# Performance work log

Measured on AMD Instinct MI355X. Metric: run time of the kernel, lower is better.

## Reference

```python
import jax, jax.numpy as jnp
import numpy as np

N, E, IN_DIM, HID, HEADS = 50000, 800000, 128, 16, 8
EPS_BN = 1e-5


def _gat_conv(x, edge_index, W, att_src, att_dst, bias, heads, out_ch, concat):
    # x: [N, F_in]; W: [heads*out_ch, F_in]; att_*: [heads, out_ch]
    n = x.shape[0]
    h = (x @ W.T).reshape(n, heads, out_ch)            # [N, H, C]
    a_src = (h * att_src[None]).sum(-1)                # [N, H]
    a_dst = (h * att_dst[None]).sum(-1)                # [N, H]
    src, dst = edge_index[0], edge_index[1]
    alpha = jax.nn.leaky_relu(a_src[src] + a_dst[dst], negative_slope=0.2)  # [E, H]
    # segment softmax over destination node (per head)
    amax = jax.ops.segment_max(alpha, dst, num_segments=n)
    amax = jnp.where(jnp.isfinite(amax), amax, 0.0)
    ex = jnp.exp(alpha - amax[dst])
    denom = jax.ops.segment_sum(ex, dst, num_segments=n)
    attn = ex / (denom[dst] + 1e-16)                   # [E, H]
    msg = h[src] * attn[:, :, None]                    # [E, H, C]
    out = jax.ops.segment_sum(msg, dst, num_segments=n)  # [N, H, C]
    out = out.reshape(n, heads * out_ch) if concat else out.mean(axis=1)
    return out + bias


def _bn_eval(h, mean, var, gamma, beta):
    return (h - mean) * jax.lax.rsqrt(var + EPS_BN) * gamma + beta


def setup_inputs() -> dict:
    key = jax.random.key(0)
    ks = jax.random.split(key, 16)
    s = 0.1
    inp = {
        "x": jax.random.normal(ks[0], (N, IN_DIM), jnp.float32),
        "edge_index": jax.random.randint(ks[1], (2, E), 0, N, jnp.int32),
        # layer 0: GATConv(128 -> 16, heads=8, concat)
        "w0": jax.random.normal(ks[2], (HEADS * HID, IN_DIM), jnp.float32) * s,
        "asrc0": jax.random.normal(ks[3], (HEADS, HID), jnp.float32) * s,
        "adst0": jax.random.normal(ks[4], (HEADS, HID), jnp.float32) * s,
        "b0": jnp.zeros((HEADS * HID,), jnp.float32),
        "skip0": jax.random.normal(ks[5], (HEADS * HID, IN_DIM), jnp.float32) * s,
        "bn0_g": jnp.ones((HEADS * HID,), jnp.float32),
        "bn0_b": jnp.zeros((HEADS * HID,), jnp.float32),
        "bn0_m": jax.random.normal(ks[6], (HEADS * HID,), jnp.float32) * s,
        "bn0_v": jax.random.uniform(ks[7], (HEADS * HID,), jnp.float32, 0.5, 1.5),
        # layer 1: GATConv(128 -> 16, heads=1, concat=False)
        "w1": jax.random.normal(ks[8], (HID, HEADS * HID), jnp.float32) * s,
        "asrc1": jax.random.normal(ks[9], (1, HID), jnp.float32) * s,
        "adst1": jax.random.normal(ks[10], (1, HID), jnp.float32) * s,
        "b1": jnp.zeros((HID,), jnp.float32),
        "skip1": jax.random.normal(ks[11], (HID, HEADS * HID), jnp.float32) * s,
        "bn1_g": jnp.ones((HID,), jnp.float32),
        "bn1_b": jnp.zeros((HID,), jnp.float32),
        "bn1_m": jax.random.normal(ks[12], (HID,), jnp.float32) * s,
        "bn1_v": jax.random.uniform(ks[13], (HID,), jnp.float32, 0.5, 1.5),
    }
    return inp


def reference(x, edge_index, w0, asrc0, adst0, b0, skip0, bn0_g, bn0_b, bn0_m, bn0_v,
              w1, asrc1, adst1, b1, skip1, bn1_g, bn1_b, bn1_m, bn1_v):
    # eval mode: dropout = identity, BN uses running stats
    h_in = x
    h = _gat_conv(h_in, edge_index, w0, asrc0, adst0, b0, HEADS, HID, True)   # [N, 128]
    h = _bn_eval(h, bn0_m, bn0_v, bn0_g, bn0_b)
    h = h + h_in @ skip0.T
    h = jax.nn.elu(h)
    h_in = h
    h = _gat_conv(h_in, edge_index, w1, asrc1, adst1, b1, 1, HID, False)      # [N, 16]
    h = _bn_eval(h, bn1_m, bn1_v, bn1_g, bn1_b)
    h = h + h_in @ skip1.T
    h = jax.nn.elu(h)
    return h
```

## Files before the change

kernel.cpp:

```cpp
#include <hip/hip_runtime.h>
#include <hip/hip_bf16.h>

#define NN 50000
#define EE 800000
#define INDIM 128
#define HIDC 16
#define NHEAD 8
#define COARSE 196
#define EPB 2048
#define CAPR 6144
#define CAPB 8192
#define CVT_BLKS 37

typedef __attribute__((ext_vector_type(8))) short bf16x8;
typedef __attribute__((ext_vector_type(4))) float f32x4;

__device__ __forceinline__ float bf2f(unsigned short u) {
    union { float f; unsigned int i; } v; v.i = ((unsigned int)u) << 16; return v.f;
}
__device__ __forceinline__ unsigned short f2bf(float f) {
    union { float f; unsigned int i; } v; v.f = f;
    unsigned int r = v.i + 0x7FFFu + ((v.i >> 16) & 1u);
    return (unsigned short)(r >> 16);
}

__global__ __launch_bounds__(256) void k_prep(
    const float* __restrict__ w0, const float* __restrict__ skip0,
    const float* __restrict__ w1, const float* __restrict__ skip1,
    const float* __restrict__ b0, const float* __restrict__ g0,
    const float* __restrict__ bb0, const float* __restrict__ m0,
    const float* __restrict__ v0,
    const float* __restrict__ b1, const float* __restrict__ g1,
    const float* __restrict__ bb1, const float* __restrict__ m1,
    const float* __restrict__ v1,
    unsigned int* __restrict__ wb2, unsigned int* __restrict__ wb1_2,
    float2* __restrict__ acb0, float2* __restrict__ acb1,
    const int* __restrict__ ei, int* __restrict__ ccur0,
    unsigned int* __restrict__ pairs)
{
    if (blockIdx.x < CVT_BLKS) {
        const long NW = 256 * 128 / 4;
        const long NW1 = 32 * 128 / 4;
        long i = (long)blockIdx.x * 256 + threadIdx.x;
        if (i < NW) {
            const float4* src = (i < 128 * 128 / 4) ? ((const float4*)w0 + i)
                                                    : ((const float4*)skip0 + (i - 128 * 128 / 4));
            float4 v = *src;
            wb2[i * 2]     = (unsigned int)f2bf(v.x) | ((unsigned int)f2bf(v.y) << 16);
            wb2[i * 2 + 1] = (unsigned int)f2bf(v.z) | ((unsigned int)f2bf(v.w) << 16);
        } else if (i < NW + NW1) {
            long j = i - NW;
            const float4* src = (j < 16 * 128 / 4) ? ((const float4*)w1 + j)
                                                   : ((const float4*)skip1 + (j - 16 * 128 / 4));
            float4 v = *src;
            wb1_2[j * 2]     = (unsigned int)f2bf(v.x) | ((unsigned int)f2bf(v.y) << 16);
            wb1_2[j * 2 + 1] = (unsigned int)f2bf(v.z) | ((unsigned int)f2bf(v.w) << 16);
        } else if (i < NW + NW1 + 128) {
            int c = (int)(i - NW - NW1);
            float A = g0[c] * rsqrtf(v0[c] + 1e-5f);
            acb0[c] = make_float2(A, (b0[c] - m0[c]) * A + bb0[c]);
        } else if (i < NW + NW1 + 128 + 16) {
            int c = (int)(i - NW - NW1 - 128);
            float A = g1[c] * rsqrtf(v1[c] + 1e-5f);
            acb1[c] = make_float2(A, (b1[c] - m1[c]) * A + bb1[c]);
        }
        return;
    }

    __shared__ int bcnt[256];
    __shared__ int lofs[256];
    __shared__ int gofs[256];
    __shared__ unsigned int stage[EPB];
    __shared__ int gpos[EPB];
    const int t = threadIdx.x;
    const int e0 = (blockIdx.x - CVT_BLKS) * EPB;

    bcnt[t] = 0;
    __syncthreads();

    int mybin[8], myrank[8];
    unsigned int mypair[8];
    #pragma unroll
    for (int k = 0; k < 8; k++) {
        int e = e0 + k * 256 + t;
        mybin[k] = -1;
        if (e < EE) {
            int s = ei[e], d = ei[EE + e];
            int b = d >> 8;
            myrank[k] = atomicAdd(&bcnt[b], 1);
            mybin[k] = b;
            mypair[k] = ((unsigned)d << 16) | (unsigned)s;
        }
    }
    __syncthreads();

    int v = bcnt[t];
    lofs[t] = v;
    __syncthreads();
    for (int off = 1; off < 256; off <<= 1) {
        int u = (t >= off) ? lofs[t - off] : 0;
        __syncthreads();
        lofs[t] += u;
        __syncthreads();
    }
    if (t < COARSE && v > 0)
        gofs[t] = t * CAPR + atomicAdd(&ccur0[t], v);
    __syncthreads();

    #pragma unroll
    for (int k = 0; k < 8; k++) {
        int b = mybin[k];
        if (b >= 0) {
            int slot = (lofs[b] - bcnt[b]) + myrank[k];
            stage[slot] = mypair[k];
            gpos[slot]  = gofs[b] + myrank[k];
        }
    }
    __syncthreads();

    const int total = lofs[255];
    for (int i = t; i < total; i += 256)
        pairs[gpos[i]] = stage[i];
}

__global__ __launch_bounds__(256) void k_mid(
    const unsigned int* __restrict__ pairs, const int* __restrict__ ccur0,
    unsigned short* __restrict__ srcidx, int* __restrict__ rowbeg,
    int* __restrict__ deg,
    const float* __restrict__ x, const unsigned short* __restrict__ wb,
    const float* __restrict__ asrc0, const float* __restrict__ adst0,
    unsigned char* __restrict__ h0f, unsigned short* __restrict__ s0b,
    float* __restrict__ a_src0, float* __restrict__ a_dst0)
{
    __shared__ int fcnt[256], fofs[256], fcur[256];
    __shared__ unsigned short stage[CAPB];

    if (blockIdx.x < COARSE) {
        const int b = blockIdx.x, t = threadIdx.x;
        const int beg = b * CAPR;
        int cnt = ccur0[b];
        if (cnt > CAPR) cnt = CAPR;

        fcnt[t] = 0;
        __syncthreads();
        for (int i = t; i < cnt; i += 256) {
            unsigned int d = pairs[beg + i] >> 16;
            atomicAdd(&fcnt[d & 255], 1);
        }
        __syncthreads();

        int v = fcnt[t];
        fofs[t] = v;
        __syncthreads();
        for (int off = 1; off < 256; off <<= 1) {
            int u = (t >= off) ? fofs[t - off] : 0;
            __syncthreads();
            fofs[t] += u;
            __syncthreads();
        }
        int ex = fofs[t] - v;
        int node = b * 256 + t;
        if (node < NN) { rowbeg[node] = beg + ex; deg[node] = v; }
        fcur[t] = ex;
        __syncthreads();

        for (int i = t; i < cnt; i += 256) {
            unsigned int p = pairs[beg + i];
            unsigned int d = p >> 16;
            int slot = atomicAdd(&fcur[d & 255], 1);
            stage[slot] = (unsigned short)(p & 0xFFFFu);
        }
        __syncthreads();
        for (int i = t; i < cnt; i += 256)
            srcidx[beg + i] = stage[i];
        return;
    }

    const int bid = blockIdx.x - COARSE;
    const int wave = threadIdx.x >> 6;
    const int lane = threadIdx.x & 63;
    const int lrow = lane & 15;
    const int quad = lane >> 4;
    const int rowbase = bid * 32;

    bf16x8 afrag[2][4];
    #pragma unroll
    for (int sub = 0; sub < 2; sub++) {
        const int row = min(rowbase + sub * 16 + lrow, NN - 1);
        const float* xr = x + (long)row * 128;
        #pragma unroll
        for (int ki = 0; ki < 4; ki++) {
            float4 a = *(const float4*)(xr + ki * 32 + quad * 8);
            float4 b = *(const float4*)(xr + ki * 32 + quad * 8 + 4);
            bf16x8 f;
            f[0] = (short)f2bf(a.x); f[1] = (short)f2bf(a.y);
            f[2] = (short)f2bf(a.z); f[3] = (short)f2bf(a.w);
            f[4] = (short)f2bf(b.x); f[5] = (short)f2bf(b.y);
            f[6] = (short)f2bf(b.z); f[7] = (short)f2bf(b.w);
            afrag[sub][ki] = f;
        }
    }

    #pragma unroll
    for (int t = 0; t < 4; t++) {
        const int jg = wave * 64 + t * 16 + lrow;
        bf16x8 bfrag[4];
        #pragma unroll
        for (int ki = 0; ki < 4; ki++)
            bfrag[ki] = *(const bf16x8*)(wb + (long)jg * 128 + ki * 32 + quad * 8);
        float4 asv = {0.f, 0.f, 0.f, 0.f}, adv = {0.f, 0.f, 0.f, 0.f};
        if (wave < 2) {
            const int cb = wave * 64 + t * 16 + quad * 4;
            asv = *(const float4*)(asrc0 + cb);
            adv = *(const float4*)(adst0 + cb);
        }
        #pragma unroll
        for (int sub = 0; sub < 2; sub++) {
            f32x4 acc = (f32x4){0.f, 0.f, 0.f, 0.f};
            #pragma unroll
            for (int ki = 0; ki < 4; ki++)
                acc = __builtin_amdgcn_mfma_f32_16x16x32_bf16(bfrag[ki], afrag[sub][ki], acc, 0, 0, 0);

            const int node = rowbase + sub * 16 + lrow;
            if (node < NN) {
                if (wave < 2) {
                    const int cb = wave * 64 + t * 16 + quad * 4;
                    unsigned int u = __builtin_amdgcn_cvt_pk_fp8_f32(acc[0], acc[1], 0u, 0);
                    u = __builtin_amdgcn_cvt_pk_fp8_f32(acc[2], acc[3], u, 1);
                    *(unsigned int*)(h0f + (long)node * 128 + cb) = u;
                    float ps = acc[0] * asv.x + acc[1] * asv.y + acc[2] * asv.z + acc[3] * asv.w;
                    float pd = acc[0] * adv.x + acc[1] * adv.y + acc[2] * adv.z + acc[3] * adv.w;
                    ps += __shfl_xor(ps, 16); ps += __shfl_xor(ps, 32);
                    pd += __shfl_xor(pd, 16); pd += __shfl_xor(pd, 32);
                    if (quad == 0) {
                        const int h = wave * 4 + t;
                        a_src0[(long)node * 8 + h] = ps;
                        a_dst0[(long)node * 8 + h] = pd;
                    }
                } else {
                    const int cb = (wave - 2) * 64 + t * 16 + quad * 4;
                    uint2 u;
                    u.x = (unsigned int)f2bf(acc[0]) | ((unsigned int)f2bf(acc[1]) << 16);
                    u.y = (unsigned int)f2bf(acc[2]) | ((unsigned int)f2bf(acc[3]) << 16);
                    *(uint2*)(s0b + (long)node * 128 + cb) = u;
                }
            }
        }
    }
}

__global__ __launch_bounds__(256) void k_agg0(
    const int* __restrict__ rowbeg, const int* __restrict__ deg,
    const unsigned short* __restrict__ srcidx,
    const unsigned char* __restrict__ h0f, const float* __restrict__ a_src0,
    const float* __restrict__ a_dst0, const unsigned short* __restrict__ s0b,
    const float2* __restrict__ acb0, unsigned int* __restrict__ hab2)
{
    const int d = (blockIdx.x * 256 + threadIdx.x) >> 6;
    if (d >= NN) return;
    const int lane = threadIdx.x & 63;
    const int beg = rowbeg[d], end = beg + deg[d];
    const int eslot = lane >> 3;
    const int hph1 = lane & 7;
    const int c = lane * 2;
    const int hsel = lane >> 3;
    const float adst = a_dst0[(long)d * 8 + hph1];

    float den = 0.f;
    float2 accA = {0.f, 0.f}, accB = {0.f, 0.f};
    for (int i = beg; i < end; i += 16) {
        const int idxA = i + eslot;
        const int idxB = i + 8 + eslot;
        const bool vA = idxA < end;
        const bool vB = idxB < end;
        const int sA = vA ? (int)srcidx[idxA] : 0;
        const int sB = vB ? (int)srcidx[idxB] : 0;
        float aA = a_src0[(long)sA * 8 + hph1] + adst;
        float aB = a_src0[(long)sB * 8 + hph1] + adst;
        aA = aA > 0.f ? aA : 0.2f * aA;
        aB = aB > 0.f ? aB : 0.2f * aB;
        const float wA = vA ? __expf(aA) : 0.f;
        const float wB = vB ? __expf(aB) : 0.f;
        den += wA + wB;
        #pragma unroll
        for (int j = 0; j < 8; j++) {
            const float wjA = __shfl(wA, j * 8 + hsel);
            const int sjA = __shfl(sA, j * 8);
            const float wjB = __shfl(wB, j * 8 + hsel);
            const int sjB = __shfl(sB, j * 8);
            const unsigned int uA = *(const unsigned short*)(h0f + (long)sjA * 128 + c);
            const unsigned int uB = *(const unsigned short*)(h0f + (long)sjB * 128 + c);
            accA.x += wjA * __builtin_amdgcn_cvt_f32_fp8(uA, 0);
            accA.y += wjA * __builtin_amdgcn_cvt_f32_fp8(uA, 1);
            accB.x += wjB * __builtin_amdgcn_cvt_f32_fp8(uB, 0);
            accB.y += wjB * __builtin_amdgcn_cvt_f32_fp8(uB, 1);
        }
    }
    float2 acc = {accA.x + accB.x, accA.y + accB.y};
    den += __shfl_xor(den, 8);
    den += __shfl_xor(den, 16);
    den += __shfl_xor(den, 32);
    const float denh = __shfl(den, hsel);
    const float inv = 1.f / (denh + 1e-16f);

    const float4 ab = *(const float4*)((const float*)acb0 + 2 * c);
    const unsigned int s0u = *(const unsigned int*)(s0b + (long)d * 128 + c);
    float x0 = acc.x * inv * ab.x + ab.y + bf2f((unsigned short)s0u);
    float x1 = acc.y * inv * ab.z + ab.w + bf2f((unsigned short)(s0u >> 16));
    x0 = x0 > 0.f ? x0 : __expf(x0) - 1.f;
    x1 = x1 > 0.f ? x1 : __expf(x1) - 1.f;
    hab2[(long)d * 64 + lane] =
        (unsigned int)f2bf(x0) | ((unsigned int)f2bf(x1) << 16);
}

__global__ __launch_bounds__(256) void k_post0(
    const unsigned short* __restrict__ hab,
    const unsigned short* __restrict__ wb1,
    const float* __restrict__ asrc1, const float* __restrict__ adst1,
    unsigned short* __restrict__ h1b, float* __restrict__ s1,
    float* __restrict__ a_src1, float* __restrict__ a_dst1)
{
    const int tid = threadIdx.x;
    const int lane = tid & 63, wave = tid >> 6;
    const int lrow = lane & 15, quad = lane >> 4;

    bf16x8 bfrag[2][4];
    #pragma unroll
    for (int t = 0; t < 2; t++)
        #pragma unroll
        for (int ki = 0; ki < 4; ki++)
            bfrag[t][ki] = *(const bf16x8*)(wb1 + (long)(t * 16 + lrow) * 128 + ki * 32 + quad * 8);
    const float avec = asrc1[lrow];
    const float dvec = adst1[lrow];

    const int tile = blockIdx.x * 4 + wave;
    if (tile * 16 >= NN) return;
    const int n0 = tile * 16;
    const long arow = (long)(n0 + lrow) * 128;

    bf16x8 afrag[4];
    #pragma unroll
    for (int ki = 0; ki < 4; ki++)
        afrag[ki] = *(const bf16x8*)(hab + arow + ki * 32 + quad * 8);

    f32x4 acc0 = (f32x4){0.f, 0.f, 0.f, 0.f};
    f32x4 acc1 = (f32x4){0.f, 0.f, 0.f, 0.f};
    #pragma unroll
    for (int ki = 0; ki < 4; ki++) {
        acc0 = __builtin_amdgcn_mfma_f32_16x16x32_bf16(afrag[ki], bfrag[0][ki], acc0, 0, 0, 0);
        acc1 = __builtin_amdgcn_mfma_f32_16x16x32_bf16(afrag[ki], bfrag[1][ki], acc1, 0, 0, 0);
    }

    #pragma unroll
    for (int r = 0; r < 4; r++) {
        const int node = n0 + quad * 4 + r;
        h1b[(long)node * 16 + lrow] = f2bf(acc0[r]);
        s1[(long)node * 16 + lrow] = acc1[r];
        float ps = acc0[r] * avec;
        float pd = acc0[r] * dvec;
        ps += __shfl_xor(ps, 1); ps += __shfl_xor(ps, 2);
        ps += __shfl_xor(ps, 4); ps += __shfl_xor(ps, 8);
        pd += __shfl_xor(pd, 1); pd += __shfl_xor(pd, 2);
        pd += __shfl_xor(pd, 4); pd += __shfl_xor(pd, 8);
        if (lrow == 0) { a_src1[node] = ps; a_dst1[node] = pd; }
    }
}

__global__ __launch_bounds__(256) void k_agg1_final(
    const int* __restrict__ rowbeg, const int* __restrict__ deg,
    const unsigned short* __restrict__ srcidx,
    const unsigned short* __restrict__ h1b, const float* __restrict__ a_src1,
    const float* __restrict__ a_dst1, const float* __restrict__ s1,
    const float2* __restrict__ acb1, float* __restrict__ out)
{
    const int gid = blockIdx.x * 256 + threadIdx.x;
    const int d = gid >> 3;
    if (d >= NN) return;
    const int lane = threadIdx.x & 63;
    const int gl = lane & 7;
    const int gb = lane & ~7;
    const int c0 = gl * 2;
    const int beg = rowbeg[d], end = beg + deg[d];
    const float adst = a_dst1[d];

    float den = 0.f;
    float2 accA = {0.f, 0.f}, accB = {0.f, 0.f};
    for (int i = beg; i < end; i += 16) {
        const int idxA = i + gl;
        const int idxB = i + 8 + gl;
        const bool vA = idxA < end;
        const bool vB = idxB < end;
        const int sA = vA ? (int)srcidx[idxA] : 0;
        const int sB = vB ? (int)srcidx[idxB] : 0;
        float aA = a_src1[sA] + adst;
        float aB = a_src1[sB] + adst;
        aA = aA > 0.f ? aA : 0.2f * aA;
        aB = aB > 0.f ? aB : 0.2f * aB;
        const float wA = vA ? __expf(aA) : 0.f;
        const float wB = vB ? __expf(aB) : 0.f;
        den += wA + wB;
        #pragma unroll
        for (int j = 0; j < 8; j++) {
            const float wjA = __shfl(wA, gb | j);
            const int sjA = __shfl(sA, gb | j);
            const float wjB = __shfl(wB, gb | j);
            const int sjB = __shfl(sB, gb | j);
            const unsigned int uA = *(const unsigned int*)(h1b + (long)sjA * 16 + c0);
            const unsigned int uB = *(const unsigned int*)(h1b + (long)sjB * 16 + c0);
            accA.x += wjA * bf2f((unsigned short)uA);
            accA.y += wjA * bf2f((unsigned short)(uA >> 16));
            accB.x += wjB * bf2f((unsigned short)uB);
            accB.y += wjB * bf2f((unsigned short)(uB >> 16));
        }
    }
    float2 acc = {accA.x + accB.x, accA.y + accB.y};
    den += __shfl_xor(den, 1);
    den += __shfl_xor(den, 2);
    den += __shfl_xor(den, 4);
    const float inv = 1.f / (den + 1e-16f);

    const float4 ab = *(const float4*)((const float*)acb1 + 2 * c0);
    float2 sv = *(const float2*)(s1 + (long)d * 16 + c0);
    float v0o = acc.x * inv * ab.x + ab.y + sv.x;
    float v1o = acc.y * inv * ab.z + ab.w + sv.y;
    v0o = v0o > 0.f ? v0o : __expf(v0o) - 1.f;
    v1o = v1o > 0.f ? v1o : __expf(v1o) - 1.f;
    *(float2*)(out + (long)d * 16 + c0) = make_float2(v0o, v1o);
}

extern "C" void kernel_launch(void* const* d_in, const int* in_sizes, int n_in,
                              void* d_out, int out_size, void* d_ws, size_t ws_size,
                              hipStream_t stream)
{
    (void)in_sizes; (void)n_in; (void)out_size; (void)ws_size;
    const float* x     = (const float*)d_in[0];
    const int*   ei    = (const int*)d_in[1];
    const float* w0    = (const float*)d_in[2];
    const float* asrc0 = (const float*)d_in[3];
    const float* adst0 = (const float*)d_in[4];
    const float* b0    = (const float*)d_in[5];
    const float* skip0 = (const float*)d_in[6];
    const float* bn0g  = (const float*)d_in[7];
    const float* bn0b  = (const float*)d_in[8];
    const float* bn0m  = (const float*)d_in[9];
    const float* bn0v  = (const float*)d_in[10];
    const float* w1    = (const float*)d_in[11];
    const float* asrc1 = (const float*)d_in[12];
    const float* adst1 = (const float*)d_in[13];
    const float* b1    = (const float*)d_in[14];
    const float* skip1 = (const float*)d_in[15];
    const float* bn1g  = (const float*)d_in[16];
    const float* bn1b  = (const float*)d_in[17];
    const float* bn1m  = (const float*)d_in[18];
    const float* bn1v  = (const float*)d_in[19];

    const long NPAIR = (long)COARSE * CAPR;
    unsigned int* pairs = (unsigned int*)d_ws;
    unsigned short* wb    = (unsigned short*)(pairs + NPAIR);
    unsigned short* wb1   = wb + 256 * 128;
    unsigned short* s0b   = wb1 + 32 * 128;
    unsigned short* hab   = s0b + (long)NN * 128;
    unsigned short* h1b   = hab + (long)NN * 128;
    unsigned short* srcidx= h1b + (long)NN * 16;
    unsigned char*  h0f   = (unsigned char*)(srcidx + NPAIR);
    float* a_src0 = (float*)(h0f + (long)NN * 128);
    float* a_dst0 = a_src0 + (long)NN * 8;
    float* s1     = a_dst0 + (long)NN * 8;
    float* a_src1 = s1 + (long)NN * 16;
    float* a_dst1 = a_src1 + NN;
    float2* acb0  = (float2*)(a_dst1 + NN);
    float2* acb1  = acb0 + 128;
    int* ccur0  = (int*)(acb1 + 16);
    int* rowbeg = ccur0 + COARSE;
    int* deg    = rowbeg + NN;

    hipMemsetAsync(ccur0, 0, (size_t)COARSE * 4, stream);

    const int PREP_BLKS = CVT_BLKS + (EE + EPB - 1) / EPB;
    k_prep<<<PREP_BLKS, 256, 0, stream>>>(
        w0, skip0, w1, skip1,
        b0, bn0g, bn0b, bn0m, bn0v, b1, bn1g, bn1b, bn1m, bn1v,
        (unsigned int*)wb, (unsigned int*)wb1, acb0, acb1,
        ei, ccur0, pairs);

    const int MID_BLKS = COARSE + (NN + 31) / 32;
    k_mid<<<MID_BLKS, 256, 0, stream>>>(
        pairs, ccur0, srcidx, rowbeg, deg,
        x, wb, asrc0, adst0, h0f, s0b, a_src0, a_dst0);

    k_agg0<<<(NN * 64 + 255) / 256, 256, 0, stream>>>(rowbeg, deg, srcidx, h0f,
                                                      a_src0, a_dst0, s0b, acb0,
                                                      (unsigned int*)hab);
    k_post0<<<(NN / 16 + 3) / 4, 256, 0, stream>>>(hab, wb1, asrc1, adst1,
                                                   h1b, s1, a_src1, a_dst1);
    k_agg1_final<<<(NN * 8 + 255) / 256, 256, 0, stream>>>(rowbeg, deg, srcidx, h1b,
                                                           a_src1, a_dst1, s1,
                                                           acb1, (float*)d_out);
}
```

Measured before the change: 206.3 us.

## Widen per-lane gather loads in both aggregation kernels with cross-lane reductions

Both edge-aggregation kernels now have each lane load 8 consecutive features per source row (uint2 of fp8 in layer 0, uint4 of bf16 in layer 1), where before each lane loaded 2. Different lane groups take different edges, and the partial sums are combined afterward with xor shuffles. This cuts the number of gather memory instructions and shuffles per edge. In exchange it adds a shuffle-reduction tail, idles three quarters of the lanes in the epilogue, and uses more accumulator registers.

New measurement: 210.5 us. +2.0%, slower.

```diff
diff --git a/kernel.cpp b/kernel.cpp
--- a/kernel.cpp
+++ b/kernel.cpp
@@ -254,7 +254,7 @@
     const unsigned short* __restrict__ srcidx,
     const unsigned char* __restrict__ h0f, const float* __restrict__ a_src0,
     const float* __restrict__ a_dst0, const unsigned short* __restrict__ s0b,
-    const float2* __restrict__ acb0, unsigned int* __restrict__ hab2)
+    const float2* __restrict__ acb0, unsigned short* __restrict__ hab)
 {
     const int d = (blockIdx.x * 256 + threadIdx.x) >> 6;
     if (d >= NN) return;
@@ -262,12 +262,14 @@
     const int beg = rowbeg[d], end = beg + deg[d];
     const int eslot = lane >> 3;
     const int hph1 = lane & 7;
-    const int c = lane * 2;
-    const int hsel = lane >> 3;
-    const float adst = a_dst0[(long)d * 8 + hph1];
+    const int l16 = lane & 15;
+    const int c0 = l16 * 8;
+    const int hsel = l16 >> 1;
+    const int q = lane >> 4;
+    const float adst = a_dst0[d * 8 + hph1];
 
     float den = 0.f;
-    float2 accA = {0.f, 0.f}, accB = {0.f, 0.f};
+    float acc[8] = {0.f, 0.f, 0.f, 0.f, 0.f, 0.f, 0.f, 0.f};
     for (int i = beg; i < end; i += 16) {
         const int idxA = i + eslot;
         const int idxB = i + 8 + eslot;
@@ -275,42 +277,67 @@
         const bool vB = idxB < end;
         const int sA = vA ? (int)srcidx[idxA] : 0;
         const int sB = vB ? (int)srcidx[idxB] : 0;
-        float aA = a_src0[(long)sA * 8 + hph1] + adst;
-        float aB = a_src0[(long)sB * 8 + hph1] + adst;
+        float aA = a_src0[sA * 8 + hph1] + adst;
+        float aB = a_src0[sB * 8 + hph1] + adst;
         aA = aA > 0.f ? aA : 0.2f * aA;
         aB = aB > 0.f ? aB : 0.2f * aB;
         const float wA = vA ? __expf(aA) : 0.f;
         const float wB = vB ? __expf(aB) : 0.f;
         den += wA + wB;
         #pragma unroll
-        for (int j = 0; j < 8; j++) {
-            const float wjA = __shfl(wA, j * 8 + hsel);
-            const int sjA = __shfl(sA, j * 8);
-            const float wjB = __shfl(wB, j * 8 + hsel);
-            const int sjB = __shfl(sB, j * 8);
-            const unsigned int uA = *(const unsigned short*)(h0f + (long)sjA * 128 + c);
-            const unsigned int uB = *(const unsigned short*)(h0f + (long)sjB * 128 + c);
-            accA.x += wjA * __builtin_amdgcn_cvt_f32_fp8(uA, 0);
-            accA.y += wjA * __builtin_amdgcn_cvt_f32_fp8(uA, 1);
-            accB.x += wjB * __builtin_amdgcn_cvt_f32_fp8(uB, 0);
-            accB.y += wjB * __builtin_amdgcn_cvt_f32_fp8(uB, 1);
-        }
-    }
-    float2 acc = {accA.x + accB.x, accA.y + accB.y};
+        for (int kk = 0; kk < 2; kk++) {
+            const int k8 = (kk * 4 + q) * 8;
+            const float wa = __shfl(wA, k8 + hsel);
+            const int   sa = __shfl(sA, k8);
+            const float wb = __shfl(wB, k8 + hsel);
+            const int   sb = __shfl(sB, k8);
+            const uint2 ua = *(const uint2*)(h0f + ((unsigned)sa << 7) + c0);
+            const uint2 ub = *(const uint2*)(h0f + ((unsigned)sb << 7) + c0);
+            acc[0] += wa * __builtin_amdgcn_cvt_f32_fp8(ua.x, 0)
+                    + wb * __builtin_amdgcn_cvt_f32_fp8(ub.x, 0);
+            acc[1] += wa * __builtin_amdgcn_cvt_f32_fp8(ua.x, 1)
+                    + wb * __builtin_amdgcn_cvt_f32_fp8(ub.x, 1);
+            acc[2] += wa * __builtin_amdgcn_cvt_f32_fp8(ua.x, 2)
+                    + wb * __builtin_amdgcn_cvt_f32_fp8(ub.x, 2);
+            acc[3] += wa * __builtin_amdgcn_cvt_f32_fp8(ua.x, 3)
+                    + wb * __builtin_amdgcn_cvt_f32_fp8(ub.x, 3);
+            acc[4] += wa * __builtin_amdgcn_cvt_f32_fp8(ua.y, 0)
+                    + wb * __builtin_amdgcn_cvt_f32_fp8(ub.y, 0);
+            acc[5] += wa * __builtin_amdgcn_cvt_f32_fp8(ua.y, 1)
+                    + wb * __builtin_amdgcn_cvt_f32_fp8(ub.y, 1);
+            acc[6] += wa * __builtin_amdgcn_cvt_f32_fp8(ua.y, 2)
+                    + wb * __builtin_amdgcn_cvt_f32_fp8(ub.y, 2);
+            acc[7] += wa * __builtin_amdgcn_cvt_f32_fp8(ua.y, 3)
+                    + wb * __builtin_amdgcn_cvt_f32_fp8(ub.y, 3);
+        }
+    }
     den += __shfl_xor(den, 8);
     den += __shfl_xor(den, 16);
     den += __shfl_xor(den, 32);
     const float denh = __shfl(den, hsel);
-    const float inv = 1.f / (denh + 1e-16f);
-
-    const float4 ab = *(const float4*)((const float*)acb0 + 2 * c);
-    const unsigned int s0u = *(const unsigned int*)(s0b + (long)d * 128 + c);
-    float x0 = acc.x * inv * ab.x + ab.y + bf2f((unsigned short)s0u);
-    float x1 = acc.y * inv * ab.z + ab.w + bf2f((unsigned short)(s0u >> 16));
-    x0 = x0 > 0.f ? x0 : __expf(x0) - 1.f;
-    x1 = x1 > 0.f ? x1 : __expf(x1) - 1.f;
-    hab2[(long)d * 64 + lane] =
-        (unsigned int)f2bf(x0) | ((unsigned int)f2bf(x1) << 16);
+    #pragma unroll
+    for (int p = 0; p < 8; p++) {
+        acc[p] += __shfl_xor(acc[p], 16);
+        acc[p] += __shfl_xor(acc[p], 32);
+    }
+
+    if (q == 0) {
+        const float inv = 1.f / (denh + 1e-16f);
+        const float4* abf = (const float4*)((const float*)acb0 + 2 * c0);
+        const uint4 su = *(const uint4*)(s0b + (long)d * 128 + c0);
+        const unsigned int sw[4] = {su.x, su.y, su.z, su.w};
+        unsigned int res[4];
+        #pragma unroll
+        for (int p = 0; p < 4; p++) {
+            const float4 ab = abf[p];
+            float x0 = acc[2 * p]     * inv * ab.x + ab.y + bf2f((unsigned short)sw[p]);
+            float x1 = acc[2 * p + 1] * inv * ab.z + ab.w + bf2f((unsigned short)(sw[p] >> 16));
+            x0 = x0 > 0.f ? x0 : __expf(x0) - 1.f;
+            x1 = x1 > 0.f ? x1 : __expf(x1) - 1.f;
+            res[p] = (unsigned int)f2bf(x0) | ((unsigned int)f2bf(x1) << 16);
+        }
+        *(uint4*)(hab + (long)d * 128 + c0) = make_uint4(res[0], res[1], res[2], res[3]);
+    }
 }
 
 __global__ __launch_bounds__(256) void k_post0(
@@ -379,12 +406,13 @@
     const int lane = threadIdx.x & 63;
     const int gl = lane & 7;
     const int gb = lane & ~7;
-    const int c0 = gl * 2;
+    const int c0 = (gl & 1) * 8;
+    const int q = gl >> 1;
     const int beg = rowbeg[d], end = beg + deg[d];
     const float adst = a_dst1[d];
 
     float den = 0.f;
-    float2 accA = {0.f, 0.f}, accB = {0.f, 0.f};
+    float acc[8] = {0.f, 0.f, 0.f, 0.f, 0.f, 0.f, 0.f, 0.f};
     for (int i = beg; i < end; i += 16) {
         const int idxA = i + gl;
         const int idxB = i + 8 + gl;
@@ -400,32 +428,51 @@
         const float wB = vB ? __expf(aB) : 0.f;
         den += wA + wB;
         #pragma unroll
-        for (int j = 0; j < 8; j++) {
-            const float wjA = __shfl(wA, gb | j);
-            const int sjA = __shfl(sA, gb | j);
-            const float wjB = __shfl(wB, gb | j);
-            const int sjB = __shfl(sB, gb | j);
-            const unsigned int uA = *(const unsigned int*)(h1b + (long)sjA * 16 + c0);
-            const unsigned int uB = *(const unsigned int*)(h1b + (long)sjB * 16 + c0);
-            accA.x += wjA * bf2f((unsigned short)uA);
-            accA.y += wjA * bf2f((unsigned short)(uA >> 16));
-            accB.x += wjB * bf2f((unsigned short)uB);
-            accB.y += wjB * bf2f((unsigned short)(uB >> 16));
-        }
-    }
-    float2 acc = {accA.x + accB.x, accA.y + accB.y};
+        for (int kk = 0; kk < 2; kk++) {
+            const int k = kk * 4 + q;
+            const float wa = __shfl(wA, gb | k);
+            const int   sa = __shfl(sA, gb | k);
+            const float wb = __shfl(wB, gb | k);
+            const int   sb = __shfl(sB, gb | k);
+            const uint4 ua = *(const uint4*)(h1b + sa * 16 + c0);
+            const uint4 ub = *(const uint4*)(h1b + sb * 16 + c0);
+            const unsigned int uw[8] = {ua.x, ua.y, ua.z, ua.w, ub.x, ub.y, ub.z, ub.w};
+            #pragma unroll
+            for (int p = 0; p < 4; p++) {
+                acc[2 * p]     += wa * bf2f((unsigned short)uw[p]);
+                acc[2 * p + 1] += wa * bf2f((unsigned short)(uw[p] >> 16));
+                acc[2 * p]     += wb * bf2f((unsigned short)uw[p + 4]);
+                acc[2 * p + 1] += wb * bf2f((unsigned short)(uw[p + 4] >> 16));
+            }
+        }
+    }
     den += __shfl_xor(den, 1);
     den += __shfl_xor(den, 2);
     den += __shfl_xor(den, 4);
-    const float inv = 1.f / (den + 1e-16f);
-
-    const float4 ab = *(const float4*)((const float*)acb1 + 2 * c0);
-    float2 sv = *(const float2*)(s1 + (long)d * 16 + c0);
-    float v0o = acc.x * inv * ab.x + ab.y + sv.x;
-    float v1o = acc.y * inv * ab.z + ab.w + sv.y;
-    v0o = v0o > 0.f ? v0o : __expf(v0o) - 1.f;
-    v1o = v1o > 0.f ? v1o : __expf(v1o) - 1.f;
-    *(float2*)(out + (long)d * 16 + c0) = make_float2(v0o, v1o);
+    #pragma unroll
+    for (int p = 0; p < 8; p++) {
+        acc[p] += __shfl_xor(acc[p], 2);
+        acc[p] += __shfl_xor(acc[p], 4);
+    }
+
+    if (q == 0) {
+        const float inv = 1.f / (den + 1e-16f);
+        const float4* abf = (const float4*)((const float*)acb1 + 2 * c0);
+        const float4 sv0 = *(const float4*)(s1 + (long)d * 16 + c0);
+        const float4 sv1 = *(const float4*)(s1 + (long)d * 16 + c0 + 4);
+        const float svf[8] = {sv0.x, sv0.y, sv0.z, sv0.w, sv1.x, sv1.y, sv1.z, sv1.w};
+        float o[8];
+        #pragma unroll
+        for (int p = 0; p < 4; p++) {
+            const float4 ab = abf[p];
+            float v0o = acc[2 * p]     * inv * ab.x + ab.y + svf[2 * p];
+            float v1o = acc[2 * p + 1] * inv * ab.z + ab.w + svf[2 * p + 1];
+            o[2 * p]     = v0o > 0.f ? v0o : __expf(v0o) - 1.f;
+            o[2 * p + 1] = v1o > 0.f ? v1o : __expf(v1o) - 1.f;
+        }
+        *(float4*)(out + (long)d * 16 + c0)     = make_float4(o[0], o[1], o[2], o[3]);
+        *(float4*)(out + (long)d * 16 + c0 + 4) = make_float4(o[4], o[5], o[6], o[7]);
+    }
 }
 
 extern "C" void kernel_launch(void* const* d_in, const int* in_sizes, int n_in,
@@ -490,7 +537,7 @@
 
     k_agg0<<<(NN * 64 + 255) / 256, 256, 0, stream>>>(rowbeg, deg, srcidx, h0f,
                                                       a_src0, a_dst0, s0b, acb0,
-                                                      (unsigned int*)hab);
+                                                      hab);
     k_post0<<<(NN / 16 + 3) / 4, 256, 0, stream>>>(hab, wb1, asrc1, adst1,
                                                    h1b, s1, a_src1, a_dst1);
     k_agg1_final<<<(NN * 8 + 255) / 256, 256, 0, stream>>>(rowbeg, deg, srcidx, h1b,
```
